# Performance work log

Hardware: AMD Instinct MI355X
Metric: run time of the kernel (lower is better)

Reference implementation:

```python
import jax, jax.numpy as jnp
import numpy as np

EMBED_DIM = 768
NUM_HEADS = 12
HEAD_DIM = EMBED_DIM // NUM_HEADS
MAX_REL = 50
B, L = 4, 1024


def setup_inputs() -> dict:
    key = jax.random.key(0)
    ks = jax.random.split(key, 8)
    query = jax.random.normal(ks[0], (B, L, EMBED_DIM), dtype=jnp.float32)
    k_in = jax.random.normal(ks[1], (B, L, EMBED_DIM), dtype=jnp.float32)
    v_in = jax.random.normal(ks[2], (B, L, EMBED_DIM), dtype=jnp.float32)
    # monotone float timestamps per batch (arange fill)
    patch_indices = jnp.arange(B * L, dtype=jnp.float32).reshape(B, L)
    std = 1.0 / np.sqrt(EMBED_DIM)
    in_proj_w = jax.random.normal(ks[3], (3 * EMBED_DIM, EMBED_DIM), dtype=jnp.float32) * std
    in_proj_b = jnp.zeros((3 * EMBED_DIM,), dtype=jnp.float32)
    out_proj_w = jax.random.normal(ks[4], (EMBED_DIM, EMBED_DIM), dtype=jnp.float32) * std
    out_proj_b = jnp.zeros((EMBED_DIM,), dtype=jnp.float32)
    rel_bias = jax.random.truncated_normal(ks[5], -2.0, 2.0, (NUM_HEADS, 2 * MAX_REL + 1), dtype=jnp.float32) * 0.1
    return {"query": query, "key": k_in, "value": v_in, "patch_indices": patch_indices,
            "in_proj_w": in_proj_w, "in_proj_b": in_proj_b,
            "out_proj_w": out_proj_w, "out_proj_b": out_proj_b, "rel_bias": rel_bias}


def _attention(query, patch_indices, in_proj_w, in_proj_b, out_proj_w, out_proj_b, rel_bias):
    Bq, Lq, D = query.shape
    H, hd, M = NUM_HEADS, HEAD_DIM, MAX_REL
    qkv = query @ in_proj_w.T + in_proj_b            # [B,L,3D]
    q, k, v = jnp.split(qkv, 3, axis=-1)
    q = q.reshape(Bq, Lq, H, hd).transpose(0, 2, 1, 3) * (hd ** -0.5)
    k = k.reshape(Bq, Lq, H, hd).transpose(0, 2, 1, 3)
    v = v.reshape(Bq, Lq, H, hd).transpose(0, 2, 1, 3)
    scores = jnp.einsum('bhld,bhmd->bhlm', q, k)     # [B,H,L,L]
    # sequence-position relative bias
    idxs = jnp.arange(Lq)
    rel_pos = jnp.clip(idxs[None, :] - idxs[:, None], -M, M) + M   # [L,L]
    scores = scores + rel_bias[:, rel_pos][None]                   # [1,H,L,L]
    # data-dependent relative-time bias
    deltas = patch_indices[:, 1:] - patch_indices[:, :-1]          # [B,L-1]
    dt = jnp.nanmedian(deltas, axis=1)
    dt = jnp.where(jnp.isfinite(dt) & (dt > 0), dt, 1.0)[:, None, None]
    rel_time = patch_indices[:, :, None] - patch_indices[:, None, :]  # [B,L,L]
    invalid = jnp.isnan(rel_time) | (rel_time < -M) | (rel_time > M)
    rel_time = jnp.where(invalid, 0.0, rel_time)
    rel_idx = (jnp.clip(jnp.round(rel_time / dt), -M, M) + M).astype(jnp.int32)  # [B,L,L]
    bias = jnp.take(rel_bias, rel_idx, axis=1)       # [H,B,L,L]
    scores = scores + jnp.moveaxis(bias, 0, 1)       # [B,H,L,L]
    probs = jax.nn.softmax(scores, axis=-1)
    out = jnp.einsum('bhlm,bhmd->bhld', probs, v)
    out = out.transpose(0, 2, 1, 3).reshape(Bq, Lq, D)
    return out @ out_proj_w.T + out_proj_b


def reference(query, key, value, patch_indices, in_proj_w, in_proj_b, out_proj_w, out_proj_b, rel_bias):
    # NOTE: the original module ignores key/value and builds qkv from query.
    return _attention(query, patch_indices, in_proj_w, in_proj_b, out_proj_w, out_proj_b, rel_bias)
```

## Files before the change

### kernel.cpp

```cpp
#include <hip/hip_runtime.h>
#include <hip/hip_bf16.h>

#define BB 4
#define LL 1024
#define DD 768
#define HH 12
#define HD 64
#define MREL 50
#define NBIAS 101
#define GK 768
#define STR 72
#define BXS 68

#define NEG_INF (-__builtin_inff())

#define QB_F   ((size_t)0)
#define KB_F   ((size_t)1572864)
#define VTB_F  ((size_t)3145728)
#define XBF_F  ((size_t)4718592)
#define WIBF_F ((size_t)6291456)
#define WOBF_F ((size_t)7176192)
#define BIDX_F ((size_t)7471104)
#define DT_F   ((size_t)9568256)

#define NQ4  (BB*LL*DD)
#define NWI4 (3*DD*DD)

typedef __attribute__((ext_vector_type(8)))  short bf16x8;
typedef __attribute__((ext_vector_type(4)))  float f32x4;
typedef __attribute__((ext_vector_type(16))) float f32x16;
typedef __attribute__((ext_vector_type(4)))  unsigned int u32x4;

__device__ __forceinline__ unsigned short f2bf(float f) {
    unsigned u = __float_as_uint(f);
    u += 0x7fffu + ((u >> 16) & 1u);
    return (unsigned short)(u >> 16);
}

__device__ __forceinline__ void gload_lds16(const void* g, void* l) {
    __builtin_amdgcn_global_load_lds(
        (const __attribute__((address_space(1))) void*)g,
        (__attribute__((address_space(3))) void*)l, 16, 0, 0);
}

__global__ __launch_bounds__(256) void prep_kernel(
    const float* __restrict__ patch, float* __restrict__ dt,
    const float* __restrict__ q, const float* __restrict__ wi, const float* __restrict__ wo,
    unsigned short* __restrict__ qd_, unsigned short* __restrict__ wid,
    unsigned short* __restrict__ wod) {
    int tid = threadIdx.x;
    if (blockIdx.x >= 4) {
        int i = ((blockIdx.x - 4) * 256 + tid) * 4;
        const float* src; unsigned short* dst; int off;
        if (i < NQ4)              { src = q;  dst = qd_; off = i; }
        else if (i < NQ4 + NWI4)  { src = wi; dst = wid; off = i - NQ4; }
        else                      { src = wo; dst = wod; off = i - NQ4 - NWI4; }
        float4 v = *(const float4*)&src[off];
        ushort4 o;
        o.x = f2bf(v.x); o.y = f2bf(v.y); o.z = f2bf(v.z); o.w = f2bf(v.w);
        *(ushort4*)&dst[off] = o;
        return;
    }
    __shared__ __align__(16) float del[1024];
    __shared__ __align__(16) unsigned long long key64[1024];
    __shared__ int nvalid;
    __shared__ float acc;
    int b = blockIdx.x;
    if (tid == 0) { nvalid = 0; acc = 0.f; }
    __syncthreads();
    int cnt = 0;
#pragma unroll
    for (int r = 0; r < 4; ++r) {
        int i = tid + r * 256;
        float v = __builtin_nanf("");
        if (i < LL - 1) {
            v = patch[b * LL + i + 1] - patch[b * LL + i];
            if (v == v) ++cnt;
        }
        del[i] = v;
        unsigned bits = (v == v) ? __float_as_uint(v) : 0x7FC00000u;
        unsigned ordk = (bits & 0x80000000u) ? ~bits : (bits | 0x80000000u);
        key64[i] = ((unsigned long long)ordk << 10) | (unsigned)i;
    }
    atomicAdd(&nvalid, cnt);
    __syncthreads();
    int i0 = tid, i1 = tid + 256, i2 = tid + 512, i3 = tid + 768;
    float v0 = del[i0], v1 = del[i1], v2 = del[i2], v3 = del[i3];
    unsigned long long k0 = key64[i0], k1 = key64[i1], k2 = key64[i2], k3 = key64[i3];
    int c0 = 0, c1 = 0, c2 = 0, c3 = 0;
#define CMPK(kx) { unsigned long long _k = (kx); \
    c0 += (_k < k0) ? 1 : 0; c1 += (_k < k1) ? 1 : 0; \
    c2 += (_k < k2) ? 1 : 0; c3 += (_k < k3) ? 1 : 0; }
    for (int j = 0; j < 1024; j += 8) {
        ulonglong2 a = *(const ulonglong2*)&key64[j];
        ulonglong2 bq = *(const ulonglong2*)&key64[j + 2];
        ulonglong2 cq = *(const ulonglong2*)&key64[j + 4];
        ulonglong2 dq = *(const ulonglong2*)&key64[j + 6];
        CMPK(a.x); CMPK(a.y); CMPK(bq.x); CMPK(bq.y);
        CMPK(cq.x); CMPK(cq.y); CMPK(dq.x); CMPK(dq.y);
    }
#undef CMPK
    int n = nvalid;
#define FIN(vr, cr) if (vr == vr) { \
    if (n & 1) { if (cr == n / 2) atomicAdd(&acc, vr); } \
    else { if (cr == n / 2 - 1 || cr == n / 2) atomicAdd(&acc, 0.5f * vr); } }
    FIN(v0, c0); FIN(v1, c1); FIN(v2, c2); FIN(v3, c3);
#undef FIN
    __syncthreads();
    if (tid == 0) {
        float m = acc;
        float res = (n > 0 && m == m && fabsf(m) != __builtin_inff() && m > 0.f) ? m : 1.0f;
        dt[b] = res;
    }
}

__global__ __launch_bounds__(256) void bidx_kernel(const float* __restrict__ patch,
                                                   const float* __restrict__ dtb,
                                                   unsigned short* __restrict__ bidx) {
    int flat = (blockIdx.x * 256 + threadIdx.x) * 8;
    int b = flat >> 20;
    int rem = flat & 1048575;
    int i = rem >> 10;
    int j0 = rem & 1023;
    float pi = patch[b * LL + i];
    float inv_dt = 1.0f / dtb[b];
    float4 pa = *(const float4*)&patch[b * LL + j0];
    float4 pb4 = *(const float4*)&patch[b * LL + j0 + 4];
    unsigned out[4];
#define MK(pj, jofs, dst, shift) { \
    int d = (j0 + jofs) - i; d = d < -MREL ? -MREL : (d > MREL ? MREL : d); \
    float rt = pi - (pj); \
    if (!(rt == rt) || rt < -(float)MREL || rt > (float)MREL) rt = 0.f; \
    float fr = fminf(fmaxf(rintf(rt * inv_dt), -(float)MREL), (float)MREL); \
    unsigned u = (unsigned)(d + MREL) | (((unsigned)((int)fr + MREL)) << 8); \
    dst |= (u << shift); }
    unsigned t;
    t = 0; MK(pa.x, 0, t, 0); MK(pa.y, 1, t, 16); out[0] = t;
    t = 0; MK(pa.z, 2, t, 0); MK(pa.w, 3, t, 16); out[1] = t;
    t = 0; MK(pb4.x, 4, t, 0); MK(pb4.y, 5, t, 16); out[2] = t;
    t = 0; MK(pb4.z, 6, t, 0); MK(pb4.w, 7, t, 16); out[3] = t;
#undef MK
    *(uint4*)&bidx[flat] = *(uint4*)&out[0];
}

#define STAGE_DB(boff, kc)                                                     \
    { _Pragma("unroll") for (int r = 0; r < 2; ++r)                            \
          gload_lds16(Ag + (size_t)(r * 32) * GK + (kc),                       \
                      smem_g + (boff) + r * 2048 + tid * 8);                   \
      _Pragma("unroll") for (int r = 0; r < 4; ++r)                            \
          gload_lds16(Bg + (size_t)(r * 32) * GK + (kc),                       \
                      smem_g + (boff) + 4096 + r * 2048 + tid * 8); }

#define GEMM_DB_MAIN()                                                         \
    __shared__ __align__(16) unsigned short smem_g[24576];                     \
    int tid = threadIdx.x;                                                     \
    int m0 = blockIdx.x << 6, n0 = blockIdx.y << 7;                            \
    int lane = tid & 63, w = tid >> 6;                                         \
    int srow = tid >> 3;                                                       \
    int scol = (((tid & 7) ^ (srow & 7)) << 3);   \
    const unsigned short* Ag = Ab + (size_t)(m0 + srow) * GK + scol;           \
    const unsigned short* Bg = Wb + (size_t)(n0 + srow) * GK + scol;           \
    f32x4 acc[4][2];                                                           \
    _Pragma("unroll") for (int i = 0; i < 4; ++i)                              \
        _Pragma("unroll") for (int j = 0; j < 2; ++j)                          \
            acc[i][j] = (f32x4){0.f, 0.f, 0.f, 0.f};                           \
    int qd_ = lane >> 4, rl = lane & 15, xA = rl & 7;                          \
    int rB = w * 32 + rl;                                                      \
    STAGE_DB(0, 0);                                                            \
    int cur = 0;                                                               \
    for (int t = 0; t < GK / 64; ++t) {                                        \
        __syncthreads();    \
        if (t + 1 < GK / 64) STAGE_DB((cur ^ 1) * 12288, (t + 1) * 64);        \
        int bo = cur * 12288;                                                  \
        const unsigned short* Abl = smem_g + bo;                               \
        const unsigned short* Bbl = smem_g + bo + 4096;                        \
        _Pragma("unroll") for (int ks = 0; ks < 2; ++ks) {                     \
            int cb = ((ks * 4 + qd_) ^ xA) << 3;        \
            bf16x8 af[4], bfr[2];                                              \
            _Pragma("unroll") for (int i = 0; i < 4; ++i)                      \
                af[i] = *(const bf16x8*)&Abl[(rl + i * 16) * 64 + cb];         \
            _Pragma("unroll") for (int j = 0; j < 2; ++j)                      \
                bfr[j] = *(const bf16x8*)&Bbl[(rB + j * 16) * 64 + cb];        \
            _Pragma("unroll") for (int i = 0; i < 4; ++i)                      \
                _Pragma("unroll") for (int j = 0; j < 2; ++j)                  \
                    acc[i][j] = __builtin_amdgcn_mfma_f32_16x16x32_bf16(       \
                        af[i], bfr[j], acc[i][j], 0, 0, 0);                    \
        }                                                                      \
        cur ^= 1;                                                              \
    }                                                                          \
    int colL = lane & 15, rq = lane >> 4;

__global__ __launch_bounds__(256) void qkv_gemm(
    const unsigned short* __restrict__ Ab, const unsigned short* __restrict__ Wb,
    const float* __restrict__ bias,
    unsigned short* __restrict__ qb, unsigned short* __restrict__ kb,
    unsigned short* __restrict__ vtb) {
    GEMM_DB_MAIN();
    int sec = n0 / DD;
    int hh0 = (n0 - sec * DD) >> 6;
    unsigned short* Ts = smem_g;
    __syncthreads();
    if (sec == 2) {
#pragma unroll
        for (int j = 0; j < 2; ++j) {
            int col_t = w * 32 + j * 16 + colL;
            float bn = bias[n0 + col_t];
#pragma unroll
            for (int i = 0; i < 4; ++i) {
                ushort4 o;
                o.x = f2bf(acc[i][j][0] + bn);
                o.y = f2bf(acc[i][j][1] + bn);
                o.z = f2bf(acc[i][j][2] + bn);
                o.w = f2bf(acc[i][j][3] + bn);
                *(ushort4*)&Ts[col_t * 72 + i * 16 + rq * 4] = o;
            }
        }
        __syncthreads();
        int nl = tid >> 1, half = tid & 1;
        int d768 = n0 + nl - 2 * DD;
        int hh = d768 >> 6, dd = d768 & 63;
        int b = m0 >> 10, l0 = (m0 & 1023) + half * 32;
        unsigned short* dst = vtb + (((size_t)b * HH + hh) * HD + dd) * LL + l0;
#pragma unroll
        for (int k = 0; k < 4; ++k)
            *(uint4*)&dst[k * 8] = *(const uint4*)&Ts[nl * 72 + half * 32 + k * 8];
    } else {
        float scale = (sec == 0) ? 0.18033688011112042f : 1.0f;
#pragma unroll
        for (int j = 0; j < 2; ++j) {
            int col_t = w * 32 + j * 16 + colL;
            float bn = bias[n0 + col_t];
#pragma unroll
            for (int i = 0; i < 4; ++i) {
                int row_t = i * 16 + rq * 4;
#pragma unroll
                for (int r = 0; r < 4; ++r)
                    Ts[(row_t + r) * 136 + col_t] = f2bf((acc[i][j][r] + bn) * scale);
            }
        }
        __syncthreads();
        int ml = tid >> 2, q4 = tid & 3;
        int b = (m0 + ml) >> 10, l = (m0 + ml) & 1023;
        unsigned short* dst = (sec == 0 ? qb : kb)
                              + (((size_t)b * HH + hh0 + (q4 >> 1)) * LL + l) * HD
                              + (q4 & 1) * 32;
#pragma unroll
        for (int k = 0; k < 4; ++k)
            *(uint4*)&dst[k * 8] = *(const uint4*)&Ts[ml * 136 + q4 * 32 + k * 8];
    }
}

__global__ __launch_bounds__(256) void out_gemm(
    const unsigned short* __restrict__ Ab, const unsigned short* __restrict__ Wb,
    const float* __restrict__ bias, float* __restrict__ C) {
    GEMM_DB_MAIN();
#pragma unroll
    for (int j = 0; j < 2; ++j) {
        int n = n0 + w * 32 + j * 16 + colL;
        float bn = bias[n];
#pragma unroll
        for (int i = 0; i < 4; ++i) {
            int rowb = m0 + i * 16 + rq * 4;
#pragma unroll
            for (int r = 0; r < 4; ++r)
                C[(size_t)(rowb + r) * DD + n] = acc[i][j][r] + bn;
        }
    }
}

__global__ __launch_bounds__(256) void attn_kernel(
    const unsigned short* __restrict__ QB, const unsigned short* __restrict__ KB,
    const unsigned short* __restrict__ VTB, const unsigned short* __restrict__ BIDX,
    const float* __restrict__ relb, unsigned short* __restrict__ aout) {
    __shared__ __align__(16) unsigned short smem[2 * 64 * STR + 64 * BXS];
    __shared__ float sb[NBIAS];
    __shared__ float psum_s[128];
    __shared__ float linv_s[64];
    unsigned short* Ks  = smem;
    unsigned short* Vt  = smem + 64 * STR;
    unsigned short* Bxs = smem + 2 * 64 * STR;
    float* fcomb = (float*)smem;

    int tid = threadIdx.x;
    int w = tid >> 6, lane = tid & 63, li = lane & 31, qd = lane >> 5;
    int jt = w & 1, it = w >> 1;
    int bh = blockIdx.x, b = bh / HH, h = bh - b * HH;
    int q0 = blockIdx.y << 6;
    if (tid < NBIAS) sb[tid] = relb[h * NBIAS + tid] * 1.44269504088896340736f;
    int i_loc = it * 32 + li;
    int i_abs = q0 + i_loc;
    bf16x8 kq[4];
    const unsigned short* qrow = QB + ((size_t)bh * LL + i_abs) * HD + qd * 8;
#pragma unroll
    for (int ks = 0; ks < 4; ++ks) kq[ks] = *(const bf16x8*)(qrow + ks * 16);
    float l_run = 0.f;
    f32x16 O0, O1;
#pragma unroll
    for (int r = 0; r < 16; ++r) { O0[r] = 0.f; O1[r] = 0.f; }
    int srow = tid >> 3, sc = (tid & 7) << 3;
    const unsigned short* kgb = KB + (size_t)bh * LL * HD;
    const unsigned short* vgb = VTB + (size_t)bh * HD * LL;
    const unsigned short* bxg = BIDX + ((size_t)b << 20) + (size_t)q0 * 1024;
    bf16x8 kvr[2], vvr[2], bxr[2];
#pragma unroll
    for (int rep = 0; rep < 2; ++rep) {
        int r = srow + rep * 32;
        kvr[rep] = *(const bf16x8*)(kgb + (size_t)r * HD + sc);
        vvr[rep] = *(const bf16x8*)(vgb + (size_t)r * LL + sc);
        bxr[rep] = *(const bf16x8*)(bxg + (size_t)r * 1024 + sc);
    }
    __syncthreads();
    float sb0 = sb[0], sb100 = sb[100];
    for (int kt = 0; kt < 16; ++kt) {
        __syncthreads();
#pragma unroll
        for (int rep = 0; rep < 2; ++rep) {
            int r = srow + rep * 32;
            *(bf16x8*)&Ks[r * STR + sc] = kvr[rep];
            *(bf16x8*)&Vt[r * STR + sc] = vvr[rep];
            *(bf16x8*)&Bxs[r * BXS + sc] = bxr[rep];
        }
        if (kt + 1 < 16) {
#pragma unroll
            for (int rep = 0; rep < 2; ++rep) {
                int r = srow + rep * 32;
                kvr[rep] = *(const bf16x8*)(kgb + (size_t)((kt + 1) * 64 + r) * HD + sc);
                vvr[rep] = *(const bf16x8*)(vgb + (size_t)r * LL + (kt + 1) * 64 + sc);
                bxr[rep] = *(const bf16x8*)(bxg + (size_t)r * 1024 + (kt + 1) * 64 + sc);
            }
        }
        __syncthreads();
        f32x16 st;
#pragma unroll
        for (int r = 0; r < 16; ++r) st[r] = 0.f;
#pragma unroll
        for (int ks = 0; ks < 4; ++ks) {
            bf16x8 ak = *(const bf16x8*)&Ks[(jt * 32 + li) * STR + ks * 16 + qd * 8];
            st = __builtin_amdgcn_mfma_f32_32x32x16_bf16(ak, kq[ks], st, 0, 0, 0);
        }
        int delta = (kt << 6) + (jt << 5) - q0 - (it << 5);
        if (delta >= 81 || delta <= -81) {
            float db = (delta >= 81) ? sb100 : sb0;
#pragma unroll
            for (int g4 = 0; g4 < 4; ++g4) {
                ushort4 bi = *(const ushort4*)&Bxs[i_loc * BXS + jt * 32 + g4 * 8 + qd * 4];
#pragma unroll
                for (int q = 0; q < 4; ++q) {
                    int r = g4 * 4 + q;
                    unsigned u = (q == 0) ? bi.x : (q == 1) ? bi.y : (q == 2) ? bi.z : bi.w;
                    st[r] = st[r] + db + sb[u >> 8];
                }
            }
        } else {
#pragma unroll
            for (int g4 = 0; g4 < 4; ++g4) {
                ushort4 bi = *(const ushort4*)&Bxs[i_loc * BXS + jt * 32 + g4 * 8 + qd * 4];
#pragma unroll
                for (int q = 0; q < 4; ++q) {
                    int r = g4 * 4 + q;
                    unsigned u = (q == 0) ? bi.x : (q == 1) ? bi.y : (q == 2) ? bi.z : bi.w;
                    st[r] = st[r] + sb[u & 0xffu] + sb[u >> 8];
                }
            }
        }
        float rs = 0.f;
        unsigned W[8];
#pragma unroll
        for (int pr = 0; pr < 8; ++pr) {
            float p0 = __builtin_amdgcn_exp2f(st[2 * pr]);
            float p1 = __builtin_amdgcn_exp2f(st[2 * pr + 1]);
            rs += p0 + p1;
            unsigned wpk;
            asm("v_cvt_pk_bf16_f32 %0, %1, %2" : "=v"(wpk) : "v"(p0), "v"(p1));
            W[pr] = wpk;
        }
        rs += __shfl_xor(rs, 32);
        l_run += rs;
        auto s02 = __builtin_amdgcn_permlane32_swap(W[0], W[2], false, false);
        auto s13 = __builtin_amdgcn_permlane32_swap(W[1], W[3], false, false);
        auto s46 = __builtin_amdgcn_permlane32_swap(W[4], W[6], false, false);
        auto s57 = __builtin_amdgcn_permlane32_swap(W[5], W[7], false, false);
        u32x4 a0w = {(unsigned)s02[0], (unsigned)s13[0], (unsigned)s02[1], (unsigned)s13[1]};
        u32x4 a1w = {(unsigned)s46[0], (unsigned)s57[0], (unsigned)s46[1], (unsigned)s57[1]};
        bf16x8 ap0 = __builtin_bit_cast(bf16x8, a0w);
        bf16x8 ap1 = __builtin_bit_cast(bf16x8, a1w);
        {
            bf16x8 bv;
            bv = *(const bf16x8*)&Vt[(li) * STR + jt * 32 + qd * 8];
            O0 = __builtin_amdgcn_mfma_f32_32x32x16_bf16(ap0, bv, O0, 0, 0, 0);
            bv = *(const bf16x8*)&Vt[(li) * STR + jt * 32 + 16 + qd * 8];
            O0 = __builtin_amdgcn_mfma_f32_32x32x16_bf16(ap1, bv, O0, 0, 0, 0);
            bv = *(const bf16x8*)&Vt[(32 + li) * STR + jt * 32 + qd * 8];
            O1 = __builtin_amdgcn_mfma_f32_32x32x16_bf16(ap0, bv, O1, 0, 0, 0);
            bv = *(const bf16x8*)&Vt[(32 + li) * STR + jt * 32 + 16 + qd * 8];
            O1 = __builtin_amdgcn_mfma_f32_32x32x16_bf16(ap1, bv, O1, 0, 0, 0);
        }
    }
    if (qd == 0) psum_s[jt * 64 + i_loc] = l_run;
    __syncthreads();
    if (jt == 0 && qd == 0)
        linv_s[i_loc] = 1.0f / (psum_s[i_loc] + psum_s[64 + i_loc]);
    if (jt == 1) {
        int ibase = it * 32;
#pragma unroll
        for (int r = 0; r < 16; ++r) {
            int irow = (r & 3) + ((r >> 2) << 3) + (qd << 2);
            fcomb[(ibase + irow) * 64 + li] = O0[r];
            fcomb[(ibase + irow) * 64 + 32 + li] = O1[r];
        }
    }
    __syncthreads();
    if (jt == 0) {
        int ibase = it * 32;
#pragma unroll
        for (int r = 0; r < 16; ++r) {
            int irow = (r & 3) + ((r >> 2) << 3) + (qd << 2);
            float inv = linv_s[ibase + irow];
            float v0 = (O0[r] + fcomb[(ibase + irow) * 64 + li]) * inv;
            float v1 = (O1[r] + fcomb[(ibase + irow) * 64 + 32 + li]) * inv;
            size_t rowoff = (size_t)(b * LL + q0 + ibase + irow) * DD + h * HD;
            aout[rowoff + li] = f2bf(v0);
            aout[rowoff + 32 + li] = f2bf(v1);
        }
    }
}

extern "C" void kernel_launch(void* const* d_in, const int* in_sizes, int n_in,
                              void* d_out, int out_size, void* d_ws, size_t ws_size,
                              hipStream_t stream) {
    const float* query    = (const float*)d_in[0];
    const float* patch    = (const float*)d_in[3];
    const float* in_w     = (const float*)d_in[4];
    const float* in_b     = (const float*)d_in[5];
    const float* out_w    = (const float*)d_in[6];
    const float* out_b    = (const float*)d_in[7];
    const float* rel_bias = (const float*)d_in[8];
    float* ws  = (float*)d_ws;
    float* out = (float*)d_out;

    unsigned short* qb   = (unsigned short*)(ws + QB_F);
    unsigned short* kb   = (unsigned short*)(ws + KB_F);
    unsigned short* vtb  = (unsigned short*)(ws + VTB_F);
    unsigned short* xbf  = (unsigned short*)(ws + XBF_F);
    unsigned short* wibf = (unsigned short*)(ws + WIBF_F);
    unsigned short* wobf = (unsigned short*)(ws + WOBF_F);
    unsigned short* bidx = (unsigned short*)(ws + BIDX_F);

    prep_kernel<<<5380, 256, 0, stream>>>(patch, ws + DT_F, query, in_w, out_w,
                                          xbf, wibf, wobf);
    bidx_kernel<<<2048, 256, 0, stream>>>(patch, ws + DT_F, bidx);
    qkv_gemm<<<dim3(64, 18), 256, 0, stream>>>(xbf, wibf, in_b, qb, kb, vtb);
    attn_kernel<<<dim3(BB * HH, LL / 64), 256, 0, stream>>>(
        qb, kb, vtb, bidx, rel_bias, xbf);
    out_gemm<<<dim3(64, 6), 256, 0, stream>>>(xbf, wobf, out_b, out);
}
```

Measured before the change: 191.4 us.

## Load attention K/V/bias tiles directly from global into registers, drop LDS staging

Removes the shared-memory staging of K, V^T and bias-index tiles, along with the two barriers per key tile. Each wave now loads its MFMA operands straight from global memory with per-lane pointers. This is meant to cut barrier and LDS round-trip overhead. In exchange, the cooperative register prefetch is lost, load latency is exposed in the loop, and data shared between waves is read redundantly from global memory and cache.

```diff
diff --git a/kernel.cpp b/kernel.cpp
--- a/kernel.cpp
+++ b/kernel.cpp
@@ -9,8 +9,6 @@
 #define MREL 50
 #define NBIAS 101
 #define GK 768
-#define STR 72
-#define BXS 68
 
 #define NEG_INF (-__builtin_inff())
 
@@ -272,14 +270,10 @@
     const unsigned short* __restrict__ QB, const unsigned short* __restrict__ KB,
     const unsigned short* __restrict__ VTB, const unsigned short* __restrict__ BIDX,
     const float* __restrict__ relb, unsigned short* __restrict__ aout) {
-    __shared__ __align__(16) unsigned short smem[2 * 64 * STR + 64 * BXS];
     __shared__ float sb[NBIAS];
     __shared__ float psum_s[128];
     __shared__ float linv_s[64];
-    unsigned short* Ks  = smem;
-    unsigned short* Vt  = smem + 64 * STR;
-    unsigned short* Bxs = smem + 2 * 64 * STR;
-    float* fcomb = (float*)smem;
+    __shared__ __align__(16) float fcomb[64 * 64];
 
     int tid = threadIdx.x;
     int w = tid >> 6, lane = tid & 63, li = lane & 31, qd = lane >> 5;
@@ -297,53 +291,41 @@
     f32x16 O0, O1;
 #pragma unroll
     for (int r = 0; r < 16; ++r) { O0[r] = 0.f; O1[r] = 0.f; }
-    int srow = tid >> 3, sc = (tid & 7) << 3;
-    const unsigned short* kgb = KB + (size_t)bh * LL * HD;
-    const unsigned short* vgb = VTB + (size_t)bh * HD * LL;
-    const unsigned short* bxg = BIDX + ((size_t)b << 20) + (size_t)q0 * 1024;
-    bf16x8 kvr[2], vvr[2], bxr[2];
-#pragma unroll
-    for (int rep = 0; rep < 2; ++rep) {
-        int r = srow + rep * 32;
-        kvr[rep] = *(const bf16x8*)(kgb + (size_t)r * HD + sc);
-        vvr[rep] = *(const bf16x8*)(vgb + (size_t)r * LL + sc);
-        bxr[rep] = *(const bf16x8*)(bxg + (size_t)r * 1024 + sc);
-    }
+
+    const unsigned short* kptr  = KB + ((size_t)bh * LL + jt * 32 + li) * HD + qd * 8;
+    const unsigned short* vptr0 = VTB + ((size_t)bh * HD + li) * LL + jt * 32 + qd * 8;
+    const unsigned short* vptr1 = VTB + ((size_t)bh * HD + 32 + li) * LL + jt * 32 + qd * 8;
+    const unsigned short* bxptr = BIDX + ((size_t)b << 20) + (size_t)(q0 + i_loc) * 1024
+                                  + jt * 32 + qd * 4;
     __syncthreads();
     float sb0 = sb[0], sb100 = sb[100];
+
     for (int kt = 0; kt < 16; ++kt) {
-        __syncthreads();
-#pragma unroll
-        for (int rep = 0; rep < 2; ++rep) {
-            int r = srow + rep * 32;
-            *(bf16x8*)&Ks[r * STR + sc] = kvr[rep];
-            *(bf16x8*)&Vt[r * STR + sc] = vvr[rep];
-            *(bf16x8*)&Bxs[r * BXS + sc] = bxr[rep];
-        }
-        if (kt + 1 < 16) {
-#pragma unroll
-            for (int rep = 0; rep < 2; ++rep) {
-                int r = srow + rep * 32;
-                kvr[rep] = *(const bf16x8*)(kgb + (size_t)((kt + 1) * 64 + r) * HD + sc);
-                vvr[rep] = *(const bf16x8*)(vgb + (size_t)r * LL + (kt + 1) * 64 + sc);
-                bxr[rep] = *(const bf16x8*)(bxg + (size_t)r * 1024 + (kt + 1) * 64 + sc);
-            }
-        }
-        __syncthreads();
+        bf16x8 ak[4];
+#pragma unroll
+        for (int ks = 0; ks < 4; ++ks)
+            ak[ks] = *(const bf16x8*)(kptr + ks * 16);
+        bf16x8 bv0a = *(const bf16x8*)(vptr0);
+        bf16x8 bv0b = *(const bf16x8*)(vptr0 + 16);
+        bf16x8 bv1a = *(const bf16x8*)(vptr1);
+        bf16x8 bv1b = *(const bf16x8*)(vptr1 + 16);
+        ushort4 bi0 = *(const ushort4*)(bxptr);
+        ushort4 bi1 = *(const ushort4*)(bxptr + 8);
+        ushort4 bi2 = *(const ushort4*)(bxptr + 16);
+        ushort4 bi3 = *(const ushort4*)(bxptr + 24);
+        kptr += 64 * HD; vptr0 += 64; vptr1 += 64; bxptr += 64;
         f32x16 st;
 #pragma unroll
         for (int r = 0; r < 16; ++r) st[r] = 0.f;
 #pragma unroll
-        for (int ks = 0; ks < 4; ++ks) {
-            bf16x8 ak = *(const bf16x8*)&Ks[(jt * 32 + li) * STR + ks * 16 + qd * 8];
-            st = __builtin_amdgcn_mfma_f32_32x32x16_bf16(ak, kq[ks], st, 0, 0, 0);
-        }
+        for (int ks = 0; ks < 4; ++ks)
+            st = __builtin_amdgcn_mfma_f32_32x32x16_bf16(ak[ks], kq[ks], st, 0, 0, 0);
         int delta = (kt << 6) + (jt << 5) - q0 - (it << 5);
         if (delta >= 81 || delta <= -81) {
             float db = (delta >= 81) ? sb100 : sb0;
 #pragma unroll
             for (int g4 = 0; g4 < 4; ++g4) {
-                ushort4 bi = *(const ushort4*)&Bxs[i_loc * BXS + jt * 32 + g4 * 8 + qd * 4];
+                ushort4 bi = (g4 == 0) ? bi0 : (g4 == 1) ? bi1 : (g4 == 2) ? bi2 : bi3;
 #pragma unroll
                 for (int q = 0; q < 4; ++q) {
                     int r = g4 * 4 + q;
@@ -354,7 +336,7 @@
         } else {
 #pragma unroll
             for (int g4 = 0; g4 < 4; ++g4) {
-                ushort4 bi = *(const ushort4*)&Bxs[i_loc * BXS + jt * 32 + g4 * 8 + qd * 4];
+                ushort4 bi = (g4 == 0) ? bi0 : (g4 == 1) ? bi1 : (g4 == 2) ? bi2 : bi3;
 #pragma unroll
                 for (int q = 0; q < 4; ++q) {
                     int r = g4 * 4 + q;
@@ -384,17 +366,10 @@
         u32x4 a1w = {(unsigned)s46[0], (unsigned)s57[0], (unsigned)s46[1], (unsigned)s57[1]};
         bf16x8 ap0 = __builtin_bit_cast(bf16x8, a0w);
         bf16x8 ap1 = __builtin_bit_cast(bf16x8, a1w);
-        {
-            bf16x8 bv;
-            bv = *(const bf16x8*)&Vt[(li) * STR + jt * 32 + qd * 8];
-            O0 = __builtin_amdgcn_mfma_f32_32x32x16_bf16(ap0, bv, O0, 0, 0, 0);
-            bv = *(const bf16x8*)&Vt[(li) * STR + jt * 32 + 16 + qd * 8];
-            O0 = __builtin_amdgcn_mfma_f32_32x32x16_bf16(ap1, bv, O0, 0, 0, 0);
-            bv = *(const bf16x8*)&Vt[(32 + li) * STR + jt * 32 + qd * 8];
-            O1 = __builtin_amdgcn_mfma_f32_32x32x16_bf16(ap0, bv, O1, 0, 0, 0);
-            bv = *(const bf16x8*)&Vt[(32 + li) * STR + jt * 32 + 16 + qd * 8];
-            O1 = __builtin_amdgcn_mfma_f32_32x32x16_bf16(ap1, bv, O1, 0, 0, 0);
-        }
+        O0 = __builtin_amdgcn_mfma_f32_32x32x16_bf16(ap0, bv0a, O0, 0, 0, 0);
+        O0 = __builtin_amdgcn_mfma_f32_32x32x16_bf16(ap1, bv0b, O0, 0, 0, 0);
+        O1 = __builtin_amdgcn_mfma_f32_32x32x16_bf16(ap0, bv1a, O1, 0, 0, 0);
+        O1 = __builtin_amdgcn_mfma_f32_32x32x16_bf16(ap1, bv1b, O1, 0, 0, 0);
     }
     if (qd == 0) psum_s[jt * 64 + i_loc] = l_run;
     __syncthreads();
```

New measurement: 225.4 us. 1.18x slower.
